# Performance work log

Hardware: AMD Instinct MI355X
Metric: run time of the kernel (lower is better)

The kernel has to match this reference:

```python
import jax, jax.numpy as jnp
import numpy as np

S, B, C = 7, 2, 80
LAMBDA_COORDS = 5.0
LAMBDA_NOOBJ = 0.5


def _iou_cxcywh(a, b):
    """Elementwise IoU of boxes in cx,cy,w,h format, shapes (..., 4) -> (...).
    Same math as torchvision box_convert(cxcywh->xyxy) + box_iou diagonal,
    computed directly (O(S^2)) instead of the O(S^4) pairwise matrix."""
    ax1 = a[..., 0] - a[..., 2] * 0.5
    ay1 = a[..., 1] - a[..., 3] * 0.5
    ax2 = a[..., 0] + a[..., 2] * 0.5
    ay2 = a[..., 1] + a[..., 3] * 0.5
    bx1 = b[..., 0] - b[..., 2] * 0.5
    by1 = b[..., 1] - b[..., 3] * 0.5
    bx2 = b[..., 0] + b[..., 2] * 0.5
    by2 = b[..., 1] + b[..., 3] * 0.5
    inter_w = jnp.clip(jnp.minimum(ax2, bx2) - jnp.maximum(ax1, bx1), 0.0)
    inter_h = jnp.clip(jnp.minimum(ay2, by2) - jnp.maximum(ay1, by1), 0.0)
    inter = inter_w * inter_h
    area_a = (ax2 - ax1) * (ay2 - ay1)
    area_b = (bx2 - bx1) * (by2 - by1)
    return inter / (area_a + area_b - inter)


def setup_inputs() -> dict:
    key = jax.random.key(0)
    k1, k2 = jax.random.split(key)
    N = 8192
    predictions = jax.random.normal(k1, (N, S, S, C + 5 * B), dtype=jnp.float32)
    target = jax.random.uniform(k2, (N, S, S, C + 5), dtype=jnp.float32)
    return {"predictions": predictions, "target": target}


def reference(predictions, target):
    preds = predictions.reshape(-1, S, S, C + 5 * B)
    target_boxes = target[..., -4:]                 # (N,S,S,4)
    pred_boxes_1 = preds[..., -4:]
    pred_boxes_2 = preds[..., -9:-5]

    iou1 = _iou_cxcywh(pred_boxes_1, target_boxes)  # (N,S,S) == diag of box_iou
    iou2 = _iou_cxcywh(pred_boxes_2, target_boxes)
    ious_idx = jnp.argmax(jnp.stack([iou1, iou2], axis=0), axis=0)  # (N,S,S)

    m1 = (1 - ious_idx).astype(preds.dtype)  # responsible-box masks
    m2 = ious_idx.astype(preds.dtype)
    obj = target[..., -5]                    # objectness (N,S,S)

    pred_boxes = obj[..., None] * (m1[..., None] * pred_boxes_1 + m2[..., None] * pred_boxes_2)

    dims = jnp.sign(pred_boxes[..., -2:]) * jnp.sqrt(jnp.abs(pred_boxes[..., -2:]) + 1e-6)
    target_dims = jnp.sqrt(target_boxes[..., -2:])

    sse = lambda a, b: jnp.sum((a - b) ** 2)  # MSELoss(reduction='sum')

    center_loss = sse(pred_boxes[..., :-3], target_boxes[..., :-3]) * LAMBDA_COORDS
    dimensions_loss = sse(dims, target_dims) * LAMBDA_COORDS
    coords_loss = center_loss + dimensions_loss

    obj_pred = preds[..., -5] * m1 + preds[..., -10] * m2
    obj_loss = sse(obj * obj_pred, obj)
    noobj_loss = sse((1.0 - obj) * obj_pred, obj) * LAMBDA_NOOBJ

    classes_loss = sse(preds[..., :-10] * obj[..., None], target[..., :-5])

    return (coords_loss, obj_loss, noobj_loss, classes_loss)
```

## Files before the change

### kernel.cpp

```cpp
#include <hip/hip_runtime.h>


#define NPRED 90
#define NTGT  85
#define NCLS  80

__device__ __forceinline__ float sgnf(float x) {
    return (x > 0.0f) ? 1.0f : ((x < 0.0f) ? -1.0f : 0.0f);
}

__device__ __forceinline__ float iou_vs_target(
    float acx, float acy, float aw, float ah,
    float bx1, float by1, float bx2, float by2, float area_b)
{
    float ax1 = acx - aw * 0.5f, ay1 = acy - ah * 0.5f;
    float ax2 = acx + aw * 0.5f, ay2 = acy + ah * 0.5f;
    float iw = fmaxf(fminf(ax2, bx2) - fmaxf(ax1, bx1), 0.0f);
    float ih = fmaxf(fminf(ay2, by2) - fmaxf(ay1, by1), 0.0f);
    float inter = iw * ih;
    float area_a = (ax2 - ax1) * (ay2 - ay1);
    return inter / (area_a + area_b - inter);
}

__global__ __launch_bounds__(256) void yolo_loss_kernel(
    const float* __restrict__ preds, const float* __restrict__ targ,
    float* __restrict__ out, int n_cells)
{
    float coords = 0.0f, objl = 0.0f, noobjl = 0.0f, clsl = 0.0f;

    int tid    = blockIdx.x * 256 + threadIdx.x;
    int stride = gridDim.x * 256;

    for (int cell = tid; cell < n_cells; cell += stride) {
        const float* p = preds + (size_t)cell * NPRED;
        const float* t = targ  + (size_t)cell * NTGT;
        const float2* p2 = (const float2*)p;

        float obj = t[NCLS];

        float cls = 0.0f;
        #pragma unroll 10
        for (int k = 0; k < NCLS / 2; ++k) {
            float2 pv = p2[k];
            float d0 = fmaf(pv.x, obj, -t[2 * k]);
            float d1 = fmaf(pv.y, obj, -t[2 * k + 1]);
            cls = fmaf(d0, d0, cls);
            cls = fmaf(d1, d1, cls);
        }
        clsl += cls;

        float2 q0 = p2[40];
        float2 q1 = p2[41];
        float2 q2 = p2[42];
        float2 q3 = p2[43];
        float2 q4 = p2[44];

        float tcx = t[81], tcy = t[82], tw = t[83], th = t[84];
        float bx1 = tcx - tw * 0.5f, by1 = tcy - th * 0.5f;
        float bx2 = tcx + tw * 0.5f, by2 = tcy + th * 0.5f;
        float area_b = (bx2 - bx1) * (by2 - by1);

        float iou1 = iou_vs_target(q3.x, q3.y, q4.x, q4.y, bx1, by1, bx2, by2, area_b);
        float iou2 = iou_vs_target(q0.y, q1.x, q1.y, q2.x, bx1, by1, bx2, by2, area_b);
        bool use2 = iou2 > iou1;

        float pcx = obj * (use2 ? q0.y : q3.x);
        float pw  = obj * (use2 ? q1.y : q4.x);
        float ph  = obj * (use2 ? q2.x : q4.y);

        float dc = pcx - tcx;
        float dw = sgnf(pw) * sqrtf(fabsf(pw) + 1e-6f) - sqrtf(tw);
        float dh = sgnf(ph) * sqrtf(fabsf(ph) + 1e-6f) - sqrtf(th);
        coords = fmaf(dc, dc, coords);
        coords = fmaf(dw, dw, coords);
        coords = fmaf(dh, dh, coords);

        float obj_pred = use2 ? q0.x : q2.y;
        float e1 = fmaf(obj, obj_pred, -obj);
        objl = fmaf(e1, e1, objl);
        float e2 = fmaf(1.0f - obj, obj_pred, -obj);
        noobjl = fmaf(e2, e2, noobjl);
    }

    #pragma unroll
    for (int off = 32; off > 0; off >>= 1) {
        coords += __shfl_down(coords, off);
        objl   += __shfl_down(objl, off);
        noobjl += __shfl_down(noobjl, off);
        clsl   += __shfl_down(clsl, off);
    }

    __shared__ float red[4][4];
    int wave = threadIdx.x >> 6;
    int lane = threadIdx.x & 63;
    if (lane == 0) {
        red[0][wave] = coords;
        red[1][wave] = objl;
        red[2][wave] = noobjl;
        red[3][wave] = clsl;
    }
    __syncthreads();
    if (threadIdx.x == 0) {
        float c = red[0][0] + red[0][1] + red[0][2] + red[0][3];
        float o = red[1][0] + red[1][1] + red[1][2] + red[1][3];
        float n = red[2][0] + red[2][1] + red[2][2] + red[2][3];
        float k = red[3][0] + red[3][1] + red[3][2] + red[3][3];
        atomicAdd(&out[0], 5.0f * c);
        atomicAdd(&out[1], o);
        atomicAdd(&out[2], 0.5f * n);
        atomicAdd(&out[3], k);
    }
}

extern "C" void kernel_launch(void* const* d_in, const int* in_sizes, int n_in,
                              void* d_out, int out_size, void* d_ws, size_t ws_size,
                              hipStream_t stream) {
    const float* preds = (const float*)d_in[0];
    const float* targ  = (const float*)d_in[1];
    float* out = (float*)d_out;

    int n_cells = in_sizes[0] / NPRED;

    hipMemsetAsync(d_out, 0, (size_t)out_size * sizeof(float), stream);

    int blocks = (n_cells + 255) / 256;
    hipLaunchKernelGGL(yolo_loss_kernel, dim3(blocks), dim3(256), 0, stream,
                       preds, targ, out, n_cells);
}
```

Measured before the change: 334.3 us.

## Stage cell tiles through shared memory with coalesced float4 loads

Each block copies a tile of 64 cells of predictions and targets into LDS using coalesced float4 global loads. Four sub-groups of 64 threads then split the 80 class terms, and sub-group 0 also computes the box and objectness terms. This replaces the earlier per-thread strided row reads, which left most of each memory transaction unused. In exchange it adds about 45KB of LDS per block, two barriers per tile and some 2-way bank conflicts on the prediction rows. The grid is also capped at a fixed persistent block count.

```diff
diff --git a/kernel.cpp b/kernel.cpp
--- a/kernel.cpp
+++ b/kernel.cpp
@@ -4,6 +4,8 @@
 #define NPRED 90
 #define NTGT  85
 #define NCLS  80
+#define TILE  64
+#define BLOCK 256
 
 __device__ __forceinline__ float sgnf(float x) {
     return (x > 0.0f) ? 1.0f : ((x < 0.0f) ? -1.0f : 0.0f);
@@ -22,64 +24,90 @@
     return inter / (area_a + area_b - inter);
 }
 
-__global__ __launch_bounds__(256) void yolo_loss_kernel(
+__global__ __launch_bounds__(BLOCK) void yolo_loss_kernel(
     const float* __restrict__ preds, const float* __restrict__ targ,
-    float* __restrict__ out, int n_cells)
+    float* __restrict__ out, int n_cells, int n_tiles)
 {
+    __shared__ __align__(16) float sp[TILE * NPRED];
+    __shared__ __align__(16) float st[TILE * NTGT];
+
     float coords = 0.0f, objl = 0.0f, noobjl = 0.0f, clsl = 0.0f;
 
-    int tid    = blockIdx.x * 256 + threadIdx.x;
-    int stride = gridDim.x * 256;
+    const int tid = threadIdx.x;
+    const int c   = tid & 63;
+    const int sub = tid >> 6;
 
-    for (int cell = tid; cell < n_cells; cell += stride) {
-        const float* p = preds + (size_t)cell * NPRED;
-        const float* t = targ  + (size_t)cell * NTGT;
-        const float2* p2 = (const float2*)p;
+    for (int tile = blockIdx.x; tile < n_tiles; tile += gridDim.x) {
+        int cell0 = tile * TILE;
+        int ncell = min(TILE, n_cells - cell0);
 
-        float obj = t[NCLS];
+        {
+            const float*  gp  = preds + (size_t)cell0 * NPRED;
+            const float4* gp4 = (const float4*)gp;
+            int nf  = ncell * NPRED;
+            int n4  = nf >> 2;
+            float4* sp4 = (float4*)sp;
+            for (int i = tid; i < n4; i += BLOCK) sp4[i] = gp4[i];
+            for (int i = (n4 << 2) + tid; i < nf; i += BLOCK) sp[i] = gp[i];
+        }
+        {
+            const float*  gt  = targ + (size_t)cell0 * NTGT;
+            const float4* gt4 = (const float4*)gt;
+            int nf  = ncell * NTGT;
+            int n4  = nf >> 2;
+            float4* st4 = (float4*)st;
+            for (int i = tid; i < n4; i += BLOCK) st4[i] = gt4[i];
+            for (int i = (n4 << 2) + tid; i < nf; i += BLOCK) st[i] = gt[i];
+        }
+        __syncthreads();
 
-        float cls = 0.0f;
-        #pragma unroll 10
-        for (int k = 0; k < NCLS / 2; ++k) {
-            float2 pv = p2[k];
-            float d0 = fmaf(pv.x, obj, -t[2 * k]);
-            float d1 = fmaf(pv.y, obj, -t[2 * k + 1]);
-            cls = fmaf(d0, d0, cls);
-            cls = fmaf(d1, d1, cls);
+        if (c < ncell) {
+            const float* pc = sp + c * NPRED;
+            const float* tc = st + c * NTGT;
+            float obj = tc[NCLS];
+
+            float cls = 0.0f;
+            int f0 = sub * 20;
+            #pragma unroll
+            for (int f = 0; f < 20; ++f) {
+                float d = fmaf(pc[f0 + f], obj, -tc[f0 + f]);
+                cls = fmaf(d, d, cls);
+            }
+            clsl += cls;
+
+            if (sub == 0) {
+                float p80 = pc[80], p81 = pc[81], p82 = pc[82], p83 = pc[83];
+                float p84 = pc[84], p85 = pc[85], p86 = pc[86], p87 = pc[87];
+                float p88 = pc[88], p89 = pc[89];
+                float tcx = tc[81], tcy = tc[82], tw = tc[83], th = tc[84];
+
+                float bx1 = tcx - tw * 0.5f, by1 = tcy - th * 0.5f;
+                float bx2 = tcx + tw * 0.5f, by2 = tcy + th * 0.5f;
+                float area_b = (bx2 - bx1) * (by2 - by1);
+
+                float iou1 = iou_vs_target(p86, p87, p88, p89, bx1, by1, bx2, by2, area_b);
+                float iou2 = iou_vs_target(p81, p82, p83, p84, bx1, by1, bx2, by2, area_b);
+                bool use2 = iou2 > iou1;
+
+                float pcx = obj * (use2 ? p81 : p86);
+                float pw  = obj * (use2 ? p83 : p88);
+                float ph  = obj * (use2 ? p84 : p89);
+
+                float dc = pcx - tcx;
+                float dw = sgnf(pw) * sqrtf(fabsf(pw) + 1e-6f) - sqrtf(tw);
+                float dh = sgnf(ph) * sqrtf(fabsf(ph) + 1e-6f) - sqrtf(th);
+                coords = fmaf(dc, dc, coords);
+                coords = fmaf(dw, dw, coords);
+                coords = fmaf(dh, dh, coords);
+
+                float obj_pred = use2 ? p80 : p85;
+                float e1 = fmaf(obj, obj_pred, -obj);
+                objl = fmaf(e1, e1, objl);
+                float e2 = fmaf(1.0f - obj, obj_pred, -obj);
+                noobjl = fmaf(e2, e2, noobjl);
+            }
         }
-        clsl += cls;
-
-        float2 q0 = p2[40];
-        float2 q1 = p2[41];
-        float2 q2 = p2[42];
-        float2 q3 = p2[43];
-        float2 q4 = p2[44];
-
-        float tcx = t[81], tcy = t[82], tw = t[83], th = t[84];
-        float bx1 = tcx - tw * 0.5f, by1 = tcy - th * 0.5f;
-        float bx2 = tcx + tw * 0.5f, by2 = tcy + th * 0.5f;
-        float area_b = (bx2 - bx1) * (by2 - by1);
-
-        float iou1 = iou_vs_target(q3.x, q3.y, q4.x, q4.y, bx1, by1, bx2, by2, area_b);
-        float iou2 = iou_vs_target(q0.y, q1.x, q1.y, q2.x, bx1, by1, bx2, by2, area_b);
-        bool use2 = iou2 > iou1;
-
-        float pcx = obj * (use2 ? q0.y : q3.x);
-        float pw  = obj * (use2 ? q1.y : q4.x);
-        float ph  = obj * (use2 ? q2.x : q4.y);
-
-        float dc = pcx - tcx;
-        float dw = sgnf(pw) * sqrtf(fabsf(pw) + 1e-6f) - sqrtf(tw);
-        float dh = sgnf(ph) * sqrtf(fabsf(ph) + 1e-6f) - sqrtf(th);
-        coords = fmaf(dc, dc, coords);
-        coords = fmaf(dw, dw, coords);
-        coords = fmaf(dh, dh, coords);
-
-        float obj_pred = use2 ? q0.x : q2.y;
-        float e1 = fmaf(obj, obj_pred, -obj);
-        objl = fmaf(e1, e1, objl);
-        float e2 = fmaf(1.0f - obj, obj_pred, -obj);
-        noobjl = fmaf(e2, e2, noobjl);
+        __syncthreads();
     }
 
     #pragma unroll
@@ -101,11 +129,11 @@
     }
     __syncthreads();
     if (threadIdx.x == 0) {
-        float c = red[0][0] + red[0][1] + red[0][2] + red[0][3];
-        float o = red[1][0] + red[1][1] + red[1][2] + red[1][3];
-        float n = red[2][0] + red[2][1] + red[2][2] + red[2][3];
-        float k = red[3][0] + red[3][1] + red[3][2] + red[3][3];
-        atomicAdd(&out[0], 5.0f * c);
+        float cd = red[0][0] + red[0][1] + red[0][2] + red[0][3];
+        float o  = red[1][0] + red[1][1] + red[1][2] + red[1][3];
+        float n  = red[2][0] + red[2][1] + red[2][2] + red[2][3];
+        float k  = red[3][0] + red[3][1] + red[3][2] + red[3][3];
+        atomicAdd(&out[0], 5.0f * cd);
         atomicAdd(&out[1], o);
         atomicAdd(&out[2], 0.5f * n);
         atomicAdd(&out[3], k);
@@ -120,10 +148,12 @@
     float* out = (float*)d_out;
 
     int n_cells = in_sizes[0] / NPRED;
+    int n_tiles = (n_cells + TILE - 1) / TILE;
 
     hipMemsetAsync(d_out, 0, (size_t)out_size * sizeof(float), stream);
 
-    int blocks = (n_cells + 255) / 256;
-    hipLaunchKernelGGL(yolo_loss_kernel, dim3(blocks), dim3(256), 0, stream,
-                       preds, targ, out, n_cells);
+    int blocks = 1568;
+    if (blocks > n_tiles) blocks = n_tiles;
+    hipLaunchKernelGGL(yolo_loss_kernel, dim3(blocks), dim3(BLOCK), 0, stream,
+                       preds, targ, out, n_cells, n_tiles);
 }
```

Result: slower. 371.5 us (+11.1%).

## Assign one wavefront per cell with coalesced lane loads and shuffles

Applied to the files above, without the earlier changes.

Replaces the thread-per-cell mapping, where each thread reads a strided 90/85-float record and global access is poorly coalesced, with a wavefront-per-cell mapping. Lanes load contiguous elements of the prediction and target rows, and box fields are broadcast by shuffles. Lane 0 does the IoU and coord math while the other lanes sit idle. The grid becomes a fixed 2048-block grid-stride loop that processes two cells per iteration to add memory-level parallelism. Memory coalescing improves, at the cost of many shuffles and divergent single-lane work per cell.

```diff
diff --git a/kernel.cpp b/kernel.cpp
--- a/kernel.cpp
+++ b/kernel.cpp
@@ -4,69 +4,63 @@
 #define NPRED 90
 #define NTGT  85
 #define NCLS  80
+#define BLOCK 256
 
 __device__ __forceinline__ float sgnf(float x) {
     return (x > 0.0f) ? 1.0f : ((x < 0.0f) ? -1.0f : 0.0f);
 }
 
-__device__ __forceinline__ float iou_vs_target(
-    float acx, float acy, float aw, float ah,
-    float bx1, float by1, float bx2, float by2, float area_b)
+struct CellLoads { float p0, p1, t0, t1; };
+
+__device__ __forceinline__ void process_cell(
+    const CellLoads& L, int lane,
+    float& coords, float& objl, float& noobjl, float& clsl)
 {
-    float ax1 = acx - aw * 0.5f, ay1 = acy - ah * 0.5f;
-    float ax2 = acx + aw * 0.5f, ay2 = acy + ah * 0.5f;
-    float iw = fmaxf(fminf(ax2, bx2) - fmaxf(ax1, bx1), 0.0f);
-    float ih = fmaxf(fminf(ay2, by2) - fmaxf(ay1, by1), 0.0f);
-    float inter = iw * ih;
-    float area_a = (ax2 - ax1) * (ay2 - ay1);
-    return inter / (area_a + area_b - inter);
-}
+    float obj = __shfl(L.t1, 16);
 
-__global__ __launch_bounds__(256) void yolo_loss_kernel(
-    const float* __restrict__ preds, const float* __restrict__ targ,
-    float* __restrict__ out, int n_cells)
-{
-    float coords = 0.0f, objl = 0.0f, noobjl = 0.0f, clsl = 0.0f;
+    float d0 = fmaf(L.p0, obj, -L.t0);
+    float acc = d0 * d0;
+    if (lane < 16) {
+        float d1 = fmaf(L.p1, obj, -L.t1);
+        acc = fmaf(d1, d1, acc);
+    }
+    clsl += acc;
 
-    int tid    = blockIdx.x * 256 + threadIdx.x;
-    int stride = gridDim.x * 256;
+    float P80 = __shfl(L.p1, 16), P81 = __shfl(L.p1, 17);
+    float P82 = __shfl(L.p1, 18), P83 = __shfl(L.p1, 19);
+    float P84 = __shfl(L.p1, 20), P85 = __shfl(L.p1, 21);
+    float P86 = __shfl(L.p1, 22);
+    float P88 = __shfl(L.p1, 24), P89 = __shfl(L.p1, 25);
+    float P87 = __shfl(L.p1, 23);
+    float tcx = __shfl(L.t1, 17), tcy = __shfl(L.t1, 18);
+    float tw  = __shfl(L.t1, 19), th  = __shfl(L.t1, 20);
 
-    for (int cell = tid; cell < n_cells; cell += stride) {
-        const float* p = preds + (size_t)cell * NPRED;
-        const float* t = targ  + (size_t)cell * NTGT;
-        const float2* p2 = (const float2*)p;
-
-        float obj = t[NCLS];
-
-        float cls = 0.0f;
-        #pragma unroll 10
-        for (int k = 0; k < NCLS / 2; ++k) {
-            float2 pv = p2[k];
-            float d0 = fmaf(pv.x, obj, -t[2 * k]);
-            float d1 = fmaf(pv.y, obj, -t[2 * k + 1]);
-            cls = fmaf(d0, d0, cls);
-            cls = fmaf(d1, d1, cls);
-        }
-        clsl += cls;
-
-        float2 q0 = p2[40];
-        float2 q1 = p2[41];
-        float2 q2 = p2[42];
-        float2 q3 = p2[43];
-        float2 q4 = p2[44];
-
-        float tcx = t[81], tcy = t[82], tw = t[83], th = t[84];
+    if (lane == 0) {
         float bx1 = tcx - tw * 0.5f, by1 = tcy - th * 0.5f;
         float bx2 = tcx + tw * 0.5f, by2 = tcy + th * 0.5f;
         float area_b = (bx2 - bx1) * (by2 - by1);
 
-        float iou1 = iou_vs_target(q3.x, q3.y, q4.x, q4.y, bx1, by1, bx2, by2, area_b);
-        float iou2 = iou_vs_target(q0.y, q1.x, q1.y, q2.x, bx1, by1, bx2, by2, area_b);
+        float ax1 = P86 - P88 * 0.5f, ay1 = P87 - P89 * 0.5f;
+        float ax2 = P86 + P88 * 0.5f, ay2 = P87 + P89 * 0.5f;
+        float iw = fmaxf(fminf(ax2, bx2) - fmaxf(ax1, bx1), 0.0f);
+        float ih = fmaxf(fminf(ay2, by2) - fmaxf(ay1, by1), 0.0f);
+        float inter1 = iw * ih;
+        float area1 = (ax2 - ax1) * (ay2 - ay1);
+        float iou1 = inter1 / (area1 + area_b - inter1);
+
+        float cx1 = P81 - P83 * 0.5f, cy1 = P82 - P84 * 0.5f;
+        float cx2 = P81 + P83 * 0.5f, cy2 = P82 + P84 * 0.5f;
+        float jw = fmaxf(fminf(cx2, bx2) - fmaxf(cx1, bx1), 0.0f);
+        float jh = fmaxf(fminf(cy2, by2) - fmaxf(cy1, by1), 0.0f);
+        float inter2 = jw * jh;
+        float area2 = (cx2 - cx1) * (cy2 - cy1);
+        float iou2 = inter2 / (area2 + area_b - inter2);
+
         bool use2 = iou2 > iou1;
 
-        float pcx = obj * (use2 ? q0.y : q3.x);
-        float pw  = obj * (use2 ? q1.y : q4.x);
-        float ph  = obj * (use2 ? q2.x : q4.y);
+        float pcx = obj * (use2 ? P81 : P86);
+        float pw  = obj * (use2 ? P83 : P88);
+        float ph  = obj * (use2 ? P84 : P89);
 
         float dc = pcx - tcx;
         float dw = sgnf(pw) * sqrtf(fabsf(pw) + 1e-6f) - sqrtf(tw);
@@ -75,11 +69,48 @@
         coords = fmaf(dw, dw, coords);
         coords = fmaf(dh, dh, coords);
 
-        float obj_pred = use2 ? q0.x : q2.y;
+        float obj_pred = use2 ? P80 : P85;
         float e1 = fmaf(obj, obj_pred, -obj);
         objl = fmaf(e1, e1, objl);
         float e2 = fmaf(1.0f - obj, obj_pred, -obj);
         noobjl = fmaf(e2, e2, noobjl);
+    }
+}
+
+__device__ __forceinline__ CellLoads load_cell(
+    const float* __restrict__ preds, const float* __restrict__ targ,
+    int c, int lane)
+{
+    const float* p = preds + (size_t)c * NPRED;
+    const float* t = targ  + (size_t)c * NTGT;
+    CellLoads L;
+    L.p0 = p[lane];
+    L.p1 = (lane < NPRED - 64) ? p[64 + lane] : 0.0f;
+    L.t0 = t[lane];
+    L.t1 = (lane < NTGT - 64) ? t[64 + lane] : 0.0f;
+    return L;
+}
+
+__global__ __launch_bounds__(BLOCK) void yolo_loss_kernel(
+    const float* __restrict__ preds, const float* __restrict__ targ,
+    float* __restrict__ out, int n_cells)
+{
+    const int lane = threadIdx.x & 63;
+    const int gw   = blockIdx.x * (BLOCK / 64) + (threadIdx.x >> 6);
+    const int W    = gridDim.x * (BLOCK / 64);
+
+    float coords = 0.0f, objl = 0.0f, noobjl = 0.0f, clsl = 0.0f;
+
+    int c = gw * 2;
+    for (; c + 1 < n_cells; c += 2 * W) {
+        CellLoads A = load_cell(preds, targ, c, lane);
+        CellLoads B = load_cell(preds, targ, c + 1, lane);
+        process_cell(A, lane, coords, objl, noobjl, clsl);
+        process_cell(B, lane, coords, objl, noobjl, clsl);
+    }
+    if (c < n_cells) {
+        CellLoads A = load_cell(preds, targ, c, lane);
+        process_cell(A, lane, coords, objl, noobjl, clsl);
     }
 
     #pragma unroll
@@ -92,7 +123,6 @@
 
     __shared__ float red[4][4];
     int wave = threadIdx.x >> 6;
-    int lane = threadIdx.x & 63;
     if (lane == 0) {
         red[0][wave] = coords;
         red[1][wave] = objl;
@@ -101,11 +131,11 @@
     }
     __syncthreads();
     if (threadIdx.x == 0) {
-        float c = red[0][0] + red[0][1] + red[0][2] + red[0][3];
-        float o = red[1][0] + red[1][1] + red[1][2] + red[1][3];
-        float n = red[2][0] + red[2][1] + red[2][2] + red[2][3];
-        float k = red[3][0] + red[3][1] + red[3][2] + red[3][3];
-        atomicAdd(&out[0], 5.0f * c);
+        float cd = red[0][0] + red[0][1] + red[0][2] + red[0][3];
+        float o  = red[1][0] + red[1][1] + red[1][2] + red[1][3];
+        float n  = red[2][0] + red[2][1] + red[2][2] + red[2][3];
+        float k  = red[3][0] + red[3][1] + red[3][2] + red[3][3];
+        atomicAdd(&out[0], 5.0f * cd);
         atomicAdd(&out[1], o);
         atomicAdd(&out[2], 0.5f * n);
         atomicAdd(&out[3], k);
@@ -123,7 +153,7 @@
 
     hipMemsetAsync(d_out, 0, (size_t)out_size * sizeof(float), stream);
 
-    int blocks = (n_cells + 255) / 256;
-    hipLaunchKernelGGL(yolo_loss_kernel, dim3(blocks), dim3(256), 0, stream,
+    int blocks = 2048;
+    hipLaunchKernelGGL(yolo_loss_kernel, dim3(blocks), dim3(BLOCK), 0, stream,
                        preds, targ, out, n_cells);
 }
```

Result: slower. 369.2 us (+10.4%).
